# Kernel optimization log

Measured on AMD Instinct MI355X. Metric: run time of the kernel, lower is better.

Reference implementation:

```python
import jax, jax.numpy as jnp
import numpy as np

B, OP, MA, F_IN, F_OUT = 8, 400, 200, 64, 64


def setup_inputs() -> dict:
    key = jax.random.key(0)
    ks = jax.random.split(key, 8)
    x = jax.random.normal(ks[0], (B, OP, F_IN), dtype=jnp.float32)
    y = jax.random.normal(ks[1], (B, MA, F_IN), dtype=jnp.float32)
    z = jax.random.normal(ks[2], (B, OP, MA, F_IN), dtype=jnp.float32)
    op_ma_adj = jax.random.randint(ks[3], (B, OP, MA), 0, 2, dtype=jnp.int32)
    # xavier-uniform-ish params
    lim = float(np.sqrt(6.0 / (F_IN + F_OUT)))
    W_op = jax.random.uniform(ks[4], (F_IN, F_OUT), minval=-lim, maxval=lim, dtype=jnp.float32)
    W_ma = jax.random.uniform(ks[5], (F_IN, F_OUT), minval=-lim, maxval=lim, dtype=jnp.float32)
    W_edge = jax.random.uniform(ks[6], (F_IN, F_OUT), minval=-lim, maxval=lim, dtype=jnp.float32)
    lim_a = float(np.sqrt(6.0 / (1 + 3 * F_OUT)))
    att_vec = jax.random.uniform(ks[7], (3 * F_OUT,), minval=-lim_a, maxval=lim_a, dtype=jnp.float32)
    return {"x": x, "y": y, "z": z, "op_ma_adj": op_ma_adj,
            "W_op": W_op, "W_ma": W_ma, "W_edge": W_edge, "att_vec": att_vec}


def reference(x, y, z, op_ma_adj, W_op, W_ma, W_edge, att_vec):
    F = W_op.shape[1]
    h_op = jnp.einsum('bni,io->bno', x, W_op)                      # [B, op, F]
    h = jnp.einsum('bmi,io->bmo', y, W_ma)                         # [B, ma, F]
    h_edge = jnp.einsum('bnmi,io->bnmo', z, W_edge).transpose(0, 2, 1, 3)  # [B, ma, op, F]
    # attention score: concat([h_op, h_ma, h_edge]) @ a  ==  per-part dot products (no BxMAxOPx3F materialization)
    a_op, a_ma, a_edge = att_vec[:F], att_vec[F:2 * F], att_vec[2 * F:]
    e = (jnp.einsum('bnf,f->bn', h_op, a_op)[:, None, :]
         + jnp.einsum('bmf,f->bm', h, a_ma)[:, :, None]
         + jnp.einsum('bmnf,f->bmn', h_edge, a_edge))              # [B, ma, op]
    e = jax.nn.leaky_relu(e, negative_slope=0.01)
    adjT = op_ma_adj.transpose(0, 2, 1)                            # [B, ma, op]
    row_empty = jnp.all(adjT == 0, axis=-1, keepdims=True)         # [B, ma, 1]
    att = jnp.where(adjT > 0, e, -jnp.inf)
    att = jnp.where(row_empty, 0.0, att)                           # empty rows -> uniform softmax (matches torch)
    att = jax.nn.softmax(att, axis=-1)                             # [B, ma, op]
    h_op_edge = h_op[:, None, :, :] + h_edge                       # [B, ma, op, F]
    h_prime = jnp.einsum('bmn,bmnf->bmf', att, h_op_edge)          # [B, ma, F]
    h_prime = jnp.where(row_empty, 0.0, h_prime) + h
    return jax.nn.elu(h_prime)
```

## Files before the change

kernel.cpp:

```cpp
#include <hip/hip_runtime.h>
#include <math.h>

#define B_   8
#define OP_  400
#define MA_  200
#define NCH  4
#define CH   100
#define RPW  25
#define PSTR 132
#define NEGM -1.0e30f

__global__ __launch_bounds__(256) void precompute_k(
    const float* __restrict__ x, const float* __restrict__ y,
    const float* __restrict__ Wop, const float* __restrict__ Wma,
    const float* __restrict__ Wedge, const float* __restrict__ att,
    float* __restrict__ ws_we, float* __restrict__ ws_eop, float* __restrict__ ws_ema)
{
    __shared__ float w_s[192];
    const int tid = threadIdx.x, wv = tid >> 6, ln = tid & 63;
    if (tid < 192) {
        const int which = tid >> 6, i = tid & 63;
        const float* W = (which == 0) ? Wop : ((which == 1) ? Wma : Wedge);
        const float* a = att + which * 64;
        float acc = 0.f;
        #pragma unroll 8
        for (int f = 0; f < 64; ++f) acc = fmaf(W[i * 64 + f], a[f], acc);
        w_s[tid] = acc;
    }
    __syncthreads();
    if (blockIdx.x == 0 && tid < 64) ws_we[tid] = w_s[128 + tid];

    const int row = blockIdx.x * 4 + wv;
    if (row < B_ * OP_) {
        float s = x[(size_t)row * 64 + ln] * w_s[ln];
        #pragma unroll
        for (int o = 32; o > 0; o >>= 1) s += __shfl_xor(s, o, 64);
        if (ln == 0) ws_eop[row] = s;
    } else if (row < B_ * OP_ + B_ * MA_) {
        const int r2 = row - B_ * OP_;
        float s = y[(size_t)r2 * 64 + ln] * w_s[64 + ln];
        #pragma unroll
        for (int o = 32; o > 0; o >>= 1) s += __shfl_xor(s, o, 64);
        if (ln == 0) ws_ema[r2] = s;
    }
}

__global__ __launch_bounds__(256) void gat_chunk(
    const float* __restrict__ x, const float* __restrict__ z,
    const int* __restrict__ adj,
    const float* __restrict__ ws_we, const float* __restrict__ ws_eop,
    const float* __restrict__ ws_ema, float* __restrict__ part)
{
    __shared__ int    act[CH];
    __shared__ float  s_arr[CH];
    __shared__ float  red[8];
    __shared__ float4 we4[16];
    __shared__ float  vred[4][64];
    __shared__ float  ured[4][64];

    const int tid = threadIdx.x, wv = tid >> 6, ln = tid & 63;
    const int blk = blockIdx.x;
    const int bm = blk / NCH, c = blk % NCH;
    const int b = bm / MA_, m = bm % MA_;
    const int n0 = c * CH;
    const int nbase = wv * RPW;

    if (tid < CH) {
        const int n = n0 + tid;
        act[tid]   = adj[((size_t)(b * OP_ + n)) * MA_ + m];
        s_arr[tid] = NEGM;
    }
    if (tid < 64) ((float*)we4)[tid] = ws_we[tid];
    const float ema = ws_ema[bm];
    __syncthreads();

    const float* zb = z + ((size_t)(b * OP_ + n0) * MA_ + m) * 64;
    const float* xb = x + (size_t)(b * OP_ + n0) * 64;

    const int r = ln >> 2, g = ln & 3;
    const float4 w0 = we4[g * 4 + 0], w1 = we4[g * 4 + 1];
    const float4 w2 = we4[g * 4 + 2], w3 = we4[g * 4 + 3];
    #pragma unroll
    for (int batch = 0; batch < 2; ++batch) {
        const int lrow = batch * 16 + r;
        const bool valid = (lrow < RPW);
        const int n = nbase + (valid ? lrow : 0);
        const bool a = valid && (act[n] != 0);
        float s = 0.f;
        if (a) {
            const float4* zr = (const float4*)(zb + (size_t)n * (MA_ * 64) + g * 16);
            float4 q0 = zr[0], q1 = zr[1], q2 = zr[2], q3 = zr[3];
            s = fmaf(q0.x, w0.x, fmaf(q0.y, w0.y, fmaf(q0.z, w0.z, q0.w * w0.w)));
            s = fmaf(q1.x, w1.x, fmaf(q1.y, w1.y, fmaf(q1.z, w1.z, fmaf(q1.w, w1.w, s))));
            s = fmaf(q2.x, w2.x, fmaf(q2.y, w2.y, fmaf(q2.z, w2.z, fmaf(q2.w, w2.w, s))));
            s = fmaf(q3.x, w3.x, fmaf(q3.y, w3.y, fmaf(q3.z, w3.z, fmaf(q3.w, w3.w, s))));
        }
        s += __shfl_xor(s, 1, 64);
        s += __shfl_xor(s, 2, 64);
        if (a && g == 0) {
            float e = s + ws_eop[b * OP_ + n0 + n] + ema;
            s_arr[n] = (e >= 0.f) ? e : 0.01f * e;
        }
    }
    __syncthreads();

    float lm = NEGM;
    for (int n = tid; n < CH; n += 256) lm = fmaxf(lm, s_arr[n]);
    #pragma unroll
    for (int o = 32; o > 0; o >>= 1) lm = fmaxf(lm, __shfl_xor(lm, o, 64));
    if (ln == 0) red[wv] = lm;
    __syncthreads();
    const float M = fmaxf(fmaxf(red[0], red[1]), fmaxf(red[2], red[3]));

    float ls = 0.f;
    for (int n = tid; n < CH; n += 256) {
        const float p = (act[n] != 0) ? __expf(s_arr[n] - M) : 0.f;
        s_arr[n] = p;
        ls += p;
    }
    #pragma unroll
    for (int o = 32; o > 0; o >>= 1) ls += __shfl_xor(ls, o, 64);
    if (ln == 0) red[4 + wv] = ls;
    __syncthreads();
    const float L = red[4] + red[5] + red[6] + red[7];

    float v = 0.f, u = 0.f;
    #pragma unroll
    for (int i = 0; i < RPW; ++i) {
        const int n = nbase + i;
        if (act[n] != 0) {
            const float p = s_arr[n];
            v = fmaf(p, zb[(size_t)n * (MA_ * 64) + ln], v);
            u = fmaf(p, xb[(size_t)n * 64 + ln], u);
        }
    }
    vred[wv][ln] = v; ured[wv][ln] = u;
    __syncthreads();

    float* pp = part + (size_t)blk * PSTR;
    if (tid < 64)        pp[tid] = vred[0][tid] + vred[1][tid] + vred[2][tid] + vred[3][tid];
    else if (tid < 128)  pp[tid] = ured[0][tid-64] + ured[1][tid-64] + ured[2][tid-64] + ured[3][tid-64];
    else if (tid == 128) { pp[128] = M; pp[129] = L; }
}

__global__ __launch_bounds__(256) void gat_combine(
    const float* __restrict__ y,
    const float* __restrict__ Wop, const float* __restrict__ Wma,
    const float* __restrict__ Wedge,
    const float* __restrict__ part, float* __restrict__ out)
{
    __shared__ float vs[4][64], us[4][64], ys[4][64];
    const int tid = threadIdx.x, wv = tid >> 6, ln = tid & 63;
    const int row = blockIdx.x * 4 + wv;

    const float* pp = part + (size_t)row * NCH * PSTR;
    float M = NEGM;
    #pragma unroll
    for (int c = 0; c < NCH; ++c) M = fmaxf(M, pp[c * PSTR + 128]);
    float L = 0.f, v = 0.f, u = 0.f;
    #pragma unroll
    for (int c = 0; c < NCH; ++c) {
        const float Mc = pp[c * PSTR + 128];
        const float w  = (Mc > -1.0e29f) ? __expf(Mc - M) : 0.f;
        L += w * pp[c * PSTR + 129];
        v += w * pp[c * PSTR + ln];
        u += w * pp[c * PSTR + 64 + ln];
    }
    const float inv = (L > 0.f) ? (1.f / L) : 0.f;
    vs[wv][ln] = v * inv;
    us[wv][ln] = u * inv;
    ys[wv][ln] = y[(size_t)row * 64 + ln];
    __syncthreads();

    float hv = 0.f;
    #pragma unroll 8
    for (int i = 0; i < 64; ++i) {
        hv += vs[wv][i] * Wedge[i * 64 + ln]
            + us[wv][i] * Wop[i * 64 + ln]
            + ys[wv][i] * Wma[i * 64 + ln];
    }
    out[(size_t)row * 64 + ln] = (hv > 0.f) ? hv : (__expf(hv) - 1.f);
}

extern "C" void kernel_launch(void* const* d_in, const int* in_sizes, int n_in,
                              void* d_out, int out_size, void* d_ws, size_t ws_size,
                              hipStream_t stream) {
    const float* x     = (const float*)d_in[0];
    const float* y     = (const float*)d_in[1];
    const float* z     = (const float*)d_in[2];
    const int*   adj   = (const int*)d_in[3];
    const float* Wop   = (const float*)d_in[4];
    const float* Wma   = (const float*)d_in[5];
    const float* Wedge = (const float*)d_in[6];
    const float* att   = (const float*)d_in[7];

    float* ws     = (float*)d_ws;
    float* ws_we  = ws;
    float* ws_eop = ws + 64;
    float* ws_ema = ws + 64 + B_ * OP_;
    float* part   = ws + 64 + B_ * OP_ + B_ * MA_;

    precompute_k<<<1200, 256, 0, stream>>>(
        x, y, Wop, Wma, Wedge, att, ws_we, ws_eop, ws_ema);
    gat_chunk<<<B_ * MA_ * NCH, 256, 0, stream>>>(
        x, z, adj, ws_we, ws_eop, ws_ema, part);
    gat_combine<<<(B_ * MA_) / 4, 256, 0, stream>>>(
        y, Wop, Wma, Wedge, part, (float*)d_out);
}
```

Before: 261.9 us.

## Assign one wavefront per 32-op chunk and precompute adjacency bitmasks

```diff
diff --git a/kernel.cpp b/kernel.cpp
--- a/kernel.cpp
+++ b/kernel.cpp
@@ -4,20 +4,42 @@
 #define B_   8
 #define OP_  400
 #define MA_  200
-#define NCH  4
-#define CH   100
-#define RPW  25
+#define NCH  13
+#define CHW  32
 #define PSTR 132
 #define NEGM -1.0e30f
+#define NW   (B_ * MA_ * NCH)
+
+typedef unsigned int u32;
 
 __global__ __launch_bounds__(256) void precompute_k(
     const float* __restrict__ x, const float* __restrict__ y,
+    const int* __restrict__ adj,
     const float* __restrict__ Wop, const float* __restrict__ Wma,
     const float* __restrict__ Wedge, const float* __restrict__ att,
-    float* __restrict__ ws_we, float* __restrict__ ws_eop, float* __restrict__ ws_ema)
+    float* __restrict__ ws_we, float* __restrict__ ws_eop,
+    float* __restrict__ ws_ema, u32* __restrict__ msk)
 {
+    const int tid = threadIdx.x, wv = tid >> 6, ln = tid & 63;
+
+    if (blockIdx.x >= 1200) {
+        const int w = (blockIdx.x - 1200) * 256 + tid;
+        if (w < NW) {
+            const int bm = w / NCH, c = w % NCH;
+            const int b = bm / MA_, m = bm % MA_;
+            u32 mk = 0;
+            #pragma unroll 8
+            for (int j = 0; j < CHW; ++j) {
+                const int n = c * CHW + j;
+                if (n < OP_ && adj[((size_t)(b * OP_ + n)) * MA_ + m] != 0)
+                    mk |= (1u << j);
+            }
+            msk[w] = mk;
+        }
+        return;
+    }
+
     __shared__ float w_s[192];
-    const int tid = threadIdx.x, wv = tid >> 6, ln = tid & 63;
     if (tid < 192) {
         const int which = tid >> 6, i = tid & 63;
         const float* W = (which == 0) ? Wop : ((which == 1) ? Wma : Wedge);
@@ -47,49 +69,38 @@
 
 __global__ __launch_bounds__(256) void gat_chunk(
     const float* __restrict__ x, const float* __restrict__ z,
-    const int* __restrict__ adj,
+    const u32* __restrict__ msk,
     const float* __restrict__ ws_we, const float* __restrict__ ws_eop,
     const float* __restrict__ ws_ema, float* __restrict__ part)
 {
-    __shared__ int    act[CH];
-    __shared__ float  s_arr[CH];
-    __shared__ float  red[8];
-    __shared__ float4 we4[16];
-    __shared__ float  vred[4][64];
-    __shared__ float  ured[4][64];
+    __shared__ float sw[4][CHW];
+    __shared__ float sp[4][CHW];
 
     const int tid = threadIdx.x, wv = tid >> 6, ln = tid & 63;
-    const int blk = blockIdx.x;
-    const int bm = blk / NCH, c = blk % NCH;
+    const int wid = blockIdx.x * 4 + wv;
+    const int bm = wid / NCH, c = wid % NCH;
     const int b = bm / MA_, m = bm % MA_;
-    const int n0 = c * CH;
-    const int nbase = wv * RPW;
-
-    if (tid < CH) {
-        const int n = n0 + tid;
-        act[tid]   = adj[((size_t)(b * OP_ + n)) * MA_ + m];
-        s_arr[tid] = NEGM;
-    }
-    if (tid < 64) ((float*)we4)[tid] = ws_we[tid];
-    const float ema = ws_ema[bm];
-    __syncthreads();
-
-    const float* zb = z + ((size_t)(b * OP_ + n0) * MA_ + m) * 64;
-    const float* xb = x + (size_t)(b * OP_ + n0) * 64;
+    const int n0 = c * CHW;
+
+    const u32 mask = msk[wid];
+    const float emav = ws_ema[bm];
 
     const int r = ln >> 2, g = ln & 3;
-    const float4 w0 = we4[g * 4 + 0], w1 = we4[g * 4 + 1];
-    const float4 w2 = we4[g * 4 + 2], w3 = we4[g * 4 + 3];
-    #pragma unroll
-    for (int batch = 0; batch < 2; ++batch) {
-        const int lrow = batch * 16 + r;
-        const bool valid = (lrow < RPW);
-        const int n = nbase + (valid ? lrow : 0);
-        const bool a = valid && (act[n] != 0);
+    const float4* wep = (const float4*)(ws_we + g * 16);
+    const float4 w0 = wep[0], w1 = wep[1], w2 = wep[2], w3 = wep[3];
+
+    const float* zrow0 = z + ((size_t)(b * OP_ + n0) * MA_ + m) * 64;
+    const float* xrow0 = x + (size_t)(b * OP_ + n0) * 64;
+
+    #pragma unroll
+    for (int bt = 0; bt < 2; ++bt) {
+        const int j = bt * 16 + r;
+        const bool a = (mask >> j) & 1u;
         float s = 0.f;
+        float res = NEGM;
         if (a) {
-            const float4* zr = (const float4*)(zb + (size_t)n * (MA_ * 64) + g * 16);
-            float4 q0 = zr[0], q1 = zr[1], q2 = zr[2], q3 = zr[3];
+            const float4* zr = (const float4*)(zrow0 + (size_t)j * (MA_ * 64) + g * 16);
+            const float4 q0 = zr[0], q1 = zr[1], q2 = zr[2], q3 = zr[3];
             s = fmaf(q0.x, w0.x, fmaf(q0.y, w0.y, fmaf(q0.z, w0.z, q0.w * w0.w)));
             s = fmaf(q1.x, w1.x, fmaf(q1.y, w1.y, fmaf(q1.z, w1.z, fmaf(q1.w, w1.w, s))));
             s = fmaf(q2.x, w2.x, fmaf(q2.y, w2.y, fmaf(q2.z, w2.z, fmaf(q2.w, w2.w, s))));
@@ -97,50 +108,43 @@
         }
         s += __shfl_xor(s, 1, 64);
         s += __shfl_xor(s, 2, 64);
-        if (a && g == 0) {
-            float e = s + ws_eop[b * OP_ + n0 + n] + ema;
-            s_arr[n] = (e >= 0.f) ? e : 0.01f * e;
-        }
-    }
-    __syncthreads();
-
-    float lm = NEGM;
-    for (int n = tid; n < CH; n += 256) lm = fmaxf(lm, s_arr[n]);
-    #pragma unroll
-    for (int o = 32; o > 0; o >>= 1) lm = fmaxf(lm, __shfl_xor(lm, o, 64));
-    if (ln == 0) red[wv] = lm;
-    __syncthreads();
-    const float M = fmaxf(fmaxf(red[0], red[1]), fmaxf(red[2], red[3]));
-
-    float ls = 0.f;
-    for (int n = tid; n < CH; n += 256) {
-        const float p = (act[n] != 0) ? __expf(s_arr[n] - M) : 0.f;
-        s_arr[n] = p;
-        ls += p;
-    }
-    #pragma unroll
-    for (int o = 32; o > 0; o >>= 1) ls += __shfl_xor(ls, o, 64);
-    if (ln == 0) red[4 + wv] = ls;
-    __syncthreads();
-    const float L = red[4] + red[5] + red[6] + red[7];
+        if (a) {
+            const float e = s + ws_eop[b * OP_ + n0 + j] + emav;
+            res = (e >= 0.f) ? e : 0.01f * e;
+        }
+        if (g == 0) sw[wv][j] = res;
+    }
+
+    const float sl = (ln < CHW) ? sw[wv][ln] : NEGM;
+    float M = sl;
+    M = fmaxf(M, __shfl_xor(M, 1, 64));
+    M = fmaxf(M, __shfl_xor(M, 2, 64));
+    M = fmaxf(M, __shfl_xor(M, 4, 64));
+    M = fmaxf(M, __shfl_xor(M, 8, 64));
+    M = fmaxf(M, __shfl_xor(M, 16, 64));
+    float p = (ln < CHW) ? __expf(sl - M) : 0.f;
+    float L = p;
+    L += __shfl_xor(L, 1, 64);
+    L += __shfl_xor(L, 2, 64);
+    L += __shfl_xor(L, 4, 64);
+    L += __shfl_xor(L, 8, 64);
+    L += __shfl_xor(L, 16, 64);
+    if (ln < CHW) sp[wv][ln] = p;
 
     float v = 0.f, u = 0.f;
     #pragma unroll
-    for (int i = 0; i < RPW; ++i) {
-        const int n = nbase + i;
-        if (act[n] != 0) {
-            const float p = s_arr[n];
-            v = fmaf(p, zb[(size_t)n * (MA_ * 64) + ln], v);
-            u = fmaf(p, xb[(size_t)n * 64 + ln], u);
-        }
-    }
-    vred[wv][ln] = v; ured[wv][ln] = u;
-    __syncthreads();
-
-    float* pp = part + (size_t)blk * PSTR;
-    if (tid < 64)        pp[tid] = vred[0][tid] + vred[1][tid] + vred[2][tid] + vred[3][tid];
-    else if (tid < 128)  pp[tid] = ured[0][tid-64] + ured[1][tid-64] + ured[2][tid-64] + ured[3][tid-64];
-    else if (tid == 128) { pp[128] = M; pp[129] = L; }
+    for (int j = 0; j < CHW; ++j) {
+        if ((mask >> j) & 1u) {
+            const float pj = sp[wv][j];
+            v = fmaf(pj, zrow0[(size_t)j * (MA_ * 64) + ln], v);
+            u = fmaf(pj, xrow0[(size_t)j * 64 + ln], u);
+        }
+    }
+
+    float* pp = part + (size_t)wid * PSTR;
+    pp[ln]      = v;
+    pp[64 + ln] = u;
+    if (ln == 0) { pp[128] = M; pp[129] = L; }
 }
 
 __global__ __launch_bounds__(256) void gat_combine(
@@ -198,12 +202,14 @@
     float* ws_we  = ws;
     float* ws_eop = ws + 64;
     float* ws_ema = ws + 64 + B_ * OP_;
-    float* part   = ws + 64 + B_ * OP_ + B_ * MA_;
-
-    precompute_k<<<1200, 256, 0, stream>>>(
-        x, y, Wop, Wma, Wedge, att, ws_we, ws_eop, ws_ema);
-    gat_chunk<<<B_ * MA_ * NCH, 256, 0, stream>>>(
-        x, z, adj, ws_we, ws_eop, ws_ema, part);
+    float* part   = ws + 4864;
+    u32*   msk    = (u32*)(ws + 4864 + (size_t)NW * PSTR);
+
+    const int maskBlocks = (NW + 255) / 256;
+    precompute_k<<<1200 + maskBlocks, 256, 0, stream>>>(
+        x, y, adj, Wop, Wma, Wedge, att, ws_we, ws_eop, ws_ema, msk);
+    gat_chunk<<<NW / 4, 256, 0, stream>>>(
+        x, z, msk, ws_we, ws_eop, ws_ema, part);
     gat_combine<<<(B_ * MA_) / 4, 256, 0, stream>>>(
         y, Wop, Wma, Wedge, part, (float*)d_out);
 }
```

New measurement: 269.0 us. 1.03x slower.
